# Kernel optimization log

Measured on AMD Instinct MI355X. Metric: run time of the kernel, lower is better.

The kernel has to match this reference:

```python
import jax, jax.numpy as jnp
import numpy as np
from jax import lax


def _make_kernel():
    # enhance_n_suppress_5x5 contour kernels: (96, 5, 5), only 4 channels non-zero
    n = 5
    k = np.zeros((96, n, n), dtype=np.float32)
    k[10] = np.array([[0, 0, 1, 0, 0], [0, 0, 1, 0, 0], [-1, -1, 0, -1, -1],
                      [0, 0, 1, 0, 0], [0, 0, 1, 0, 0]], np.float32) / 8.0
    k[5] = np.array([[0, 0, -1, 0, 0], [0, 0, -1, 0, 0], [1, 1, 0, 1, 1],
                     [0, 0, -1, 0, 0], [0, 0, -1, 0, 0]], np.float32) / 8.0
    diag = np.array([[1, 0, 0, 0, -1], [0, 1, 0, -1, 0], [0, 0, 0, 0, 0],
                     [0, -1, 0, 1, 0], [-1, 0, 0, 0, 1]], np.float32) / 8.0
    k[54] = diag
    k[67] = diag
    return jnp.asarray(k)


def setup_inputs() -> dict:
    key = jax.random.key(0)
    x = jax.random.normal(key, (128, 55, 55, 96), dtype=jnp.float32)  # NHWC
    kernel = _make_kernel()  # (96, 5, 5)
    return {"x": x, "kernel": kernel}


def reference(x, kernel):
    # Depthwise 5x5 correlation per channel + residual (same math as the
    # python double loop of slice+batch_dot in the original layer).
    ch = x.shape[-1]
    # (96,5,5) -> HWIO depthwise kernel (5,5,1,96)
    k = jnp.transpose(kernel, (1, 2, 0))[:, :, None, :]
    y = lax.conv_general_dilated(
        x, k,
        window_strides=(1, 1),
        padding="SAME",
        dimension_numbers=("NHWC", "HWIO", "NHWC"),
        feature_group_count=ch,
    )
    return x + y
```

## Files before the change

kernel.cpp:

```cpp
#include <hip/hip_runtime.h>

#define NB 128
#define HW 55
#define IMG (HW * HW)
#define CH 96
#define GROUPS 24
#define TAPS 25
#define NPIX (NB * IMG)
#define RSTRIP 5
#define NSTRIP (HW / RSTRIP)
#define NWG (NB * NSTRIP)
#define SROWS (RSTRIP + 4)
#define GCHUNK 4
#define SLOTG 32
#define NXCD 8
#define BITEMS (RSTRIP * HW * GROUPS)
#define SPIX (RSTRIP * HW)
#define STAGEN (SROWS * HW)

typedef float v4f __attribute__((ext_vector_type(4)));


__global__ void repack_kernel(const float* __restrict__ k,
                              float4* __restrict__ wslot,
                              int2* __restrict__ dslot,
                              int* __restrict__ tapflag,
                              int* __restrict__ gact,
                              int* __restrict__ nga,
                              int* __restrict__ nspad) {
    __shared__ int s_ns[GROUPS];
    int g = threadIdx.x;
    if (g < GROUPS) {
        int ns = 0;
        for (int tap = 0; tap < TAPS; ++tap) {
            float w0 = k[(4 * g + 0) * TAPS + tap];
            float w1 = k[(4 * g + 1) * TAPS + tap];
            float w2 = k[(4 * g + 2) * TAPS + tap];
            float w3 = k[(4 * g + 3) * TAPS + tap];
            if (w0 != 0.f || w1 != 0.f || w2 != 0.f || w3 != 0.f) {
                int dh = tap / 5 - 2, dw = tap % 5 - 2;
                wslot[g * SLOTG + ns] = make_float4(w0, w1, w2, w3);
                dslot[g * SLOTG + ns] = make_int2(dh + 2, dw);
                ++ns;
            }
        }
        for (int s = ns; s < SLOTG; ++s) {
            wslot[g * SLOTG + s] = make_float4(0.f, 0.f, 0.f, 0.f);
            dslot[g * SLOTG + s] = make_int2(2, 0);
        }
        tapflag[g] = (ns > 0) ? 1 : 0;
        s_ns[g] = ns;
    }
    __syncthreads();
    if (threadIdx.x == 0) {
        int na = 0, m = 0;
        for (int gg = 0; gg < GROUPS; ++gg)
            if (s_ns[gg] > 0) { gact[na++] = gg; m = m > s_ns[gg] ? m : s_ns[gg]; }
        *nga = na;
        *nspad = (m + 7) & ~7;
    }
}

__global__ __launch_bounds__(256) void tiled_kernel(const float* __restrict__ x,
                                                    const float4* __restrict__ wslot,
                                                    const int2* __restrict__ dslot,
                                                    const int* __restrict__ tapflag,
                                                    const int* __restrict__ gact,
                                                    const int* __restrict__ p_nga,
                                                    const int* __restrict__ p_nspad,
                                                    float* __restrict__ out) {
    __shared__ v4f s_x[GCHUNK * STAGEN];
    __shared__ v4f s_cv[GCHUNK * SPIX];
    __shared__ float4 s_w[GCHUNK * 8];
    __shared__ int s_d[GCHUNK * 8];
    __shared__ int s_info[GROUPS];
    __shared__ int s_gg[GCHUNK];

    const int q = NWG / NXCD, r = NWG % NXCD;
    int xcd = blockIdx.x & (NXCD - 1);
    int bidx = blockIdx.x >> 3;
    int swz = (xcd < r ? xcd * (q + 1) : r * (q + 1) + (xcd - r) * q) + bidx;

    const int n = swz / NSTRIP;
    const int strip = swz % NSTRIP;
    const int h0 = strip * RSTRIP;
    const int tid = threadIdx.x;
    const int nga = *p_nga;
    const int nsb = (*p_nspad) >> 3;
    const int base_f4 = (n * IMG + h0 * HW) * GROUPS;
    const v4f* x4 = (const v4f*)x;
    v4f* o4 = (v4f*)out;

    int nchunk = (nga + GCHUNK - 1) / GCHUNK;
    if (nchunk < 1) nchunk = 1;
    const bool single = (nchunk == 1);

    for (int c = 0; c < nchunk; ++c) {
        const int c0 = c * GCHUNK;
        int cn = nga - c0;
        if (cn > GCHUNK) cn = GCHUNK;
        if (cn < 0) cn = 0;

        if (tid < GROUPS) s_info[tid] = tapflag[tid] ? -2 : -1;
        __syncthreads();
        if (tid < cn) { s_info[gact[c0 + tid]] = tid; s_gg[tid] = gact[c0 + tid]; }
        if (tid < cn * 8) {
            int ci = tid >> 3, s = tid & 7;
            int gg = gact[c0 + ci];
            s_w[tid] = wslot[gg * SLOTG + s];
            int2 dd = dslot[gg * SLOTG + s];
            s_d[tid] = (dd.x << 8) | (dd.y + 2);
        }
        const int stcnt = STAGEN * cn;
        const int wcn = HW * cn;
        for (int i = tid; i < stcnt; i += 256) {
            int srow = i / wcn;
            int rem2 = i - srow * wcn;
            int pix = rem2 / cn;
            int ci = rem2 - pix * cn;
            int h = h0 - 2 + srow;
            v4f v = {0.f, 0.f, 0.f, 0.f};
            if ((unsigned)h < (unsigned)HW)
                v = x4[(n * IMG + h * HW + pix) * GROUPS + gact[c0 + ci]];
            s_x[ci * STAGEN + srow * HW + pix] = v;
        }
        __syncthreads();

        const int acnt = cn * SPIX;
        for (int j = tid; j < acnt; j += 256) {
            int ci = j / SPIX;
            int pixrel = j - ci * SPIX;
            int rr = pixrel / HW;
            int pix = pixrel - rr * HW;
            const v4f* sxg = s_x + ci * STAGEN;
            v4f acc = {0.f, 0.f, 0.f, 0.f};
#pragma unroll
            for (int si = 0; si < 8; ++si) {
                int d = s_d[ci * 8 + si];
                int srow = rr + (d >> 8);
                int pix2 = pix + (d & 255) - 2;
                bool valid = (unsigned)pix2 < (unsigned)HW;
                float sc = valid ? 1.f : 0.f;
                int p2 = valid ? pix2 : 0;
                v4f xv = sxg[srow * HW + p2];
                float4 wv = s_w[ci * 8 + si];
                acc.x += (wv.x * sc) * xv.x;
                acc.y += (wv.y * sc) * xv.y;
                acc.z += (wv.z * sc) * xv.z;
                acc.w += (wv.w * sc) * xv.w;
            }
            for (int sb = 1; sb < nsb; ++sb) {
                int gg = s_gg[ci];
#pragma unroll
                for (int si = 0; si < 8; ++si) {
                    int s = sb * 8 + si;
                    int2 dd = dslot[gg * SLOTG + s];
                    int srow = rr + dd.x;
                    int pix2 = pix + dd.y;
                    bool valid = (unsigned)pix2 < (unsigned)HW;
                    float sc = valid ? 1.f : 0.f;
                    int p2 = valid ? pix2 : 0;
                    v4f xv = sxg[srow * HW + p2];
                    float4 wv = wslot[gg * SLOTG + s];
                    acc.x += (wv.x * sc) * xv.x;
                    acc.y += (wv.y * sc) * xv.y;
                    acc.z += (wv.z * sc) * xv.z;
                    acc.w += (wv.w * sc) * xv.w;
                }
            }
            s_cv[ci * SPIX + pixrel] = acc;
        }
        __syncthreads();

        for (int i = tid; i < BITEMS; i += 256) {
            int pixrel = i / GROUPS;
            int gout = i - pixrel * GROUPS;
            v4f acc = x4[base_f4 + i];
            int gidx = s_info[gout];
            if (gidx >= 0) {
                v4f cv = s_cv[gidx * SPIX + pixrel];
                acc.x += cv.x; acc.y += cv.y; acc.z += cv.z; acc.w += cv.w;
            }
            bool dostore = single || (gidx >= 0) || (c == 0 && gidx == -1);
            if (dostore)
                __builtin_nontemporal_store(acc, &o4[base_f4 + i]);
        }
        if (c + 1 < nchunk) __syncthreads();
    }
}

__global__ __launch_bounds__(256) void fallback_kernel(const float* __restrict__ x,
                                                       const float* __restrict__ kraw,
                                                       float* __restrict__ out) {
    int t = blockIdx.x * 256 + threadIdx.x;
    if (t >= NPIX * GROUPS) return;
    int g = t % GROUPS;
    int pixel = t / GROUPS;
    int rem = pixel % IMG;
    int h = rem / HW;
    int w = rem - h * HW;
    int base = pixel * CH + g * 4;
    const float4 xc = *reinterpret_cast<const float4*>(x + base);
    float4 acc = make_float4(xc.x, xc.y, xc.z, xc.w);
#pragma unroll
    for (int dh = -2; dh <= 2; ++dh)
#pragma unroll
        for (int dw = -2; dw <= 2; ++dw) {
            const int tap = (dh + 2) * 5 + (dw + 2);
            const bool valid = ((unsigned)(h + dh) < (unsigned)HW) &
                               ((unsigned)(w + dw) < (unsigned)HW);
            const float vs = valid ? 1.0f : 0.0f;
            const int off = valid ? (dh * HW * CH + dw * CH) : 0;
            const float4 xv = *reinterpret_cast<const float4*>(x + base + off);
            acc.x += (kraw[(g * 4 + 0) * TAPS + tap] * vs) * xv.x;
            acc.y += (kraw[(g * 4 + 1) * TAPS + tap] * vs) * xv.y;
            acc.z += (kraw[(g * 4 + 2) * TAPS + tap] * vs) * xv.z;
            acc.w += (kraw[(g * 4 + 3) * TAPS + tap] * vs) * xv.w;
        }
    *reinterpret_cast<float4*>(out + base) = acc;
}

extern "C" void kernel_launch(void* const* d_in, const int* in_sizes, int n_in,
                              void* d_out, int out_size, void* d_ws, size_t ws_size,
                              hipStream_t stream) {
    const float* x = (const float*)d_in[0];
    const float* k = (const float*)d_in[1];
    float* out = (float*)d_out;

    const size_t sz_wslot = (size_t)GROUPS * SLOTG * sizeof(float4);
    const size_t sz_dslot = (size_t)GROUPS * SLOTG * sizeof(int2);
    const size_t sz_flag = GROUPS * sizeof(int);
    const size_t sz_gact = GROUPS * sizeof(int);
    const size_t ws_need = sz_wslot + sz_dslot + sz_flag + sz_gact + 2 * sizeof(int);

    if (ws_size >= ws_need) {
        char* p = (char*)d_ws;
        float4* wslot = (float4*)p;  p += sz_wslot;
        int2* dslot = (int2*)p;      p += sz_dslot;
        int* tapflag = (int*)p;      p += sz_flag;
        int* gact = (int*)p;         p += sz_gact;
        int* nga = (int*)p;          p += sizeof(int);
        int* nspad = (int*)p;

        repack_kernel<<<1, 64, 0, stream>>>(k, wslot, dslot, tapflag, gact, nga, nspad);
        tiled_kernel<<<NWG, 256, 0, stream>>>(x, wslot, dslot, tapflag, gact,
                                              nga, nspad, out);
    } else {
        const int blocks = (NPIX * GROUPS) / 256;
        fallback_kernel<<<blocks, 256, 0, stream>>>(x, k, out);
    }
}
```

Measured before the change: 90.14 us.

## Split conv and residual stages into pixel sub-chunks to shrink LDS buffer

```diff
diff --git a/kernel.cpp b/kernel.cpp
--- a/kernel.cpp
+++ b/kernel.cpp
@@ -17,6 +17,7 @@
 #define BITEMS (RSTRIP * HW * GROUPS)
 #define SPIX (RSTRIP * HW)
 #define STAGEN (SROWS * HW)
+#define PCH 128
 
 typedef float v4f __attribute__((ext_vector_type(4)));
 
@@ -70,7 +71,7 @@
                                                     const int* __restrict__ p_nspad,
                                                     float* __restrict__ out) {
     __shared__ v4f s_x[GCHUNK * STAGEN];
-    __shared__ v4f s_cv[GCHUNK * SPIX];
+    __shared__ v4f s_cv[GCHUNK * PCH];
     __shared__ float4 s_w[GCHUNK * 8];
     __shared__ int s_d[GCHUNK * 8];
     __shared__ int s_info[GROUPS];
@@ -126,66 +127,88 @@
         }
         __syncthreads();
 
-        const int acnt = cn * SPIX;
-        for (int j = tid; j < acnt; j += 256) {
-            int ci = j / SPIX;
-            int pixrel = j - ci * SPIX;
-            int rr = pixrel / HW;
-            int pix = pixrel - rr * HW;
-            const v4f* sxg = s_x + ci * STAGEN;
-            v4f acc = {0.f, 0.f, 0.f, 0.f};
-#pragma unroll
-            for (int si = 0; si < 8; ++si) {
-                int d = s_d[ci * 8 + si];
-                int srow = rr + (d >> 8);
-                int pix2 = pix + (d & 255) - 2;
-                bool valid = (unsigned)pix2 < (unsigned)HW;
-                float sc = valid ? 1.f : 0.f;
-                int p2 = valid ? pix2 : 0;
-                v4f xv = sxg[srow * HW + p2];
-                float4 wv = s_w[ci * 8 + si];
-                acc.x += (wv.x * sc) * xv.x;
-                acc.y += (wv.y * sc) * xv.y;
-                acc.z += (wv.z * sc) * xv.z;
-                acc.w += (wv.w * sc) * xv.w;
-            }
-            for (int sb = 1; sb < nsb; ++sb) {
-                int gg = s_gg[ci];
-#pragma unroll
-                for (int si = 0; si < 8; ++si) {
-                    int s = sb * 8 + si;
-                    int2 dd = dslot[gg * SLOTG + s];
-                    int srow = rr + dd.x;
-                    int pix2 = pix + dd.y;
-                    bool valid = (unsigned)pix2 < (unsigned)HW;
-                    float sc = valid ? 1.f : 0.f;
-                    int p2 = valid ? pix2 : 0;
-                    v4f xv = sxg[srow * HW + p2];
-                    float4 wv = wslot[gg * SLOTG + s];
-                    acc.x += (wv.x * sc) * xv.x;
-                    acc.y += (wv.y * sc) * xv.y;
-                    acc.z += (wv.z * sc) * xv.z;
-                    acc.w += (wv.w * sc) * xv.w;
+        for (int p0 = 0; p0 < SPIX; p0 += PCH) {
+            int pcn = SPIX - p0;
+            if (pcn > PCH) pcn = PCH;
+
+            for (int j = tid; j < cn * PCH; j += 256) {
+                int ci = j >> 7;
+                int pixrel = j & (PCH - 1);
+                if (pixrel < pcn) {
+                    int pa = p0 + pixrel;
+                    int rr = pa / HW;
+                    int pix = pa - rr * HW;
+                    const v4f* sxg = s_x + ci * STAGEN;
+                    v4f acc = {0.f, 0.f, 0.f, 0.f};
+#pragma unroll
+                    for (int si = 0; si < 8; ++si) {
+                        int d = s_d[ci * 8 + si];
+                        int srow = rr + (d >> 8);
+                        int pix2 = pix + (d & 255) - 2;
+                        bool valid = (unsigned)pix2 < (unsigned)HW;
+                        float sc = valid ? 1.f : 0.f;
+                        int p2 = valid ? pix2 : 0;
+                        v4f xv = sxg[srow * HW + p2];
+                        float4 wv = s_w[ci * 8 + si];
+                        acc.x += (wv.x * sc) * xv.x;
+                        acc.y += (wv.y * sc) * xv.y;
+                        acc.z += (wv.z * sc) * xv.z;
+                        acc.w += (wv.w * sc) * xv.w;
+                    }
+                    for (int sb = 1; sb < nsb; ++sb) {
+                        int gg = s_gg[ci];
+#pragma unroll
+                        for (int si = 0; si < 8; ++si) {
+                            int s = sb * 8 + si;
+                            int2 dd = dslot[gg * SLOTG + s];
+                            int srow = rr + dd.x;
+                            int pix2 = pix + dd.y;
+                            bool valid = (unsigned)pix2 < (unsigned)HW;
+                            float sc = valid ? 1.f : 0.f;
+                            int p2 = valid ? pix2 : 0;
+                            v4f xv = sxg[srow * HW + p2];
+                            float4 wv = wslot[gg * SLOTG + s];
+                            acc.x += (wv.x * sc) * xv.x;
+                            acc.y += (wv.y * sc) * xv.y;
+                            acc.z += (wv.z * sc) * xv.z;
+                            acc.w += (wv.w * sc) * xv.w;
+                        }
+                    }
+                    s_cv[ci * PCH + pixrel] = acc;
                 }
             }
-            s_cv[ci * SPIX + pixrel] = acc;
-        }
-        __syncthreads();
-
-        for (int i = tid; i < BITEMS; i += 256) {
-            int pixrel = i / GROUPS;
-            int gout = i - pixrel * GROUPS;
-            v4f acc = x4[base_f4 + i];
-            int gidx = s_info[gout];
-            if (gidx >= 0) {
-                v4f cv = s_cv[gidx * SPIX + pixrel];
-                acc.x += cv.x; acc.y += cv.y; acc.z += cv.z; acc.w += cv.w;
+            __syncthreads();
+
+            const int ib = base_f4 + p0 * GROUPS;
+            if (pcn == PCH) {
+                for (int jj = tid; jj < 768; jj += 256) {
+#pragma unroll
+                    for (int kc = 0; kc < 4; ++kc) {
+                        int i = jj + kc * 768;
+                        int pr = i / GROUPS;
+                        int gout = i - pr * GROUPS;
+                        v4f acc = x4[ib + i];
+                        int gidx = s_info[gout];
+                        if (gidx >= 0) acc += s_cv[gidx * PCH + pr];
+                        if (single || gidx >= 0 || (c == 0 && gidx == -1))
+                            __builtin_nontemporal_store(acc, &o4[ib + i]);
+                    }
+                }
+            } else {
+                const int tot = pcn * GROUPS;
+                for (int i = tid; i < tot; i += 256) {
+                    int pr = i / GROUPS;
+                    int gout = i - pr * GROUPS;
+                    v4f acc = x4[ib + i];
+                    int gidx = s_info[gout];
+                    if (gidx >= 0) acc += s_cv[gidx * PCH + pr];
+                    if (single || gidx >= 0 || (c == 0 && gidx == -1))
+                        __builtin_nontemporal_store(acc, &o4[ib + i]);
+                }
             }
-            bool dostore = single || (gidx >= 0) || (c == 0 && gidx == -1);
-            if (dostore)
-                __builtin_nontemporal_store(acc, &o4[base_f4 + i]);
-        }
-        if (c + 1 < nchunk) __syncthreads();
+            if (p0 + PCH < SPIX || c + 1 < nchunk)
+                __syncthreads();
+        }
     }
 }
 
```

Result: slower. 94.58 us (+4.9%).

## Split fused tiled kernel into conv-to-buffer pass and streaming residual pass

Applied to the files above, without the earlier changes.

```diff
diff --git a/kernel.cpp b/kernel.cpp
--- a/kernel.cpp
+++ b/kernel.cpp
@@ -9,14 +9,17 @@
 #define NPIX (NB * IMG)
 #define RSTRIP 5
 #define NSTRIP (HW / RSTRIP)
-#define NWG (NB * NSTRIP)
+#define NWG1 (NB * NSTRIP)
+#define TOTALF4 (NPIX * GROUPS)
+#define NWG2 (TOTALF4 / 256)
 #define SROWS (RSTRIP + 4)
 #define GCHUNK 4
 #define SLOTG 32
 #define NXCD 8
-#define BITEMS (RSTRIP * HW * GROUPS)
 #define SPIX (RSTRIP * HW)
 #define STAGEN (SROWS * HW)
+#define BITEMS (RSTRIP * HW * GROUPS)
+#define PCH_FB 128
 
 typedef float v4f __attribute__((ext_vector_type(4)));
 
@@ -27,7 +30,8 @@
                               int* __restrict__ tapflag,
                               int* __restrict__ gact,
                               int* __restrict__ nga,
-                              int* __restrict__ nspad) {
+                              int* __restrict__ nspad,
+                              int* __restrict__ amask) {
     __shared__ int s_ns[GROUPS];
     int g = threadIdx.x;
     if (g < GROUPS) {
@@ -53,30 +57,36 @@
     }
     __syncthreads();
     if (threadIdx.x == 0) {
-        int na = 0, m = 0;
+        int na = 0, m = 0, msk = 0;
         for (int gg = 0; gg < GROUPS; ++gg)
-            if (s_ns[gg] > 0) { gact[na++] = gg; m = m > s_ns[gg] ? m : s_ns[gg]; }
+            if (s_ns[gg] > 0) {
+                gact[na++] = gg;
+                msk |= (1 << gg);
+                m = m > s_ns[gg] ? m : s_ns[gg];
+            }
         *nga = na;
         *nspad = (m + 7) & ~7;
-    }
-}
-
-__global__ __launch_bounds__(256) void tiled_kernel(const float* __restrict__ x,
-                                                    const float4* __restrict__ wslot,
-                                                    const int2* __restrict__ dslot,
-                                                    const int* __restrict__ tapflag,
-                                                    const int* __restrict__ gact,
-                                                    const int* __restrict__ p_nga,
-                                                    const int* __restrict__ p_nspad,
-                                                    float* __restrict__ out) {
+        *amask = msk;
+    }
+}
+
+__global__ __launch_bounds__(256) void conv_kernel(const float* __restrict__ x,
+                                                   const float4* __restrict__ wslot,
+                                                   const int2* __restrict__ dslot,
+                                                   const int* __restrict__ gact,
+                                                   const int* __restrict__ p_nga,
+                                                   const int* __restrict__ p_nspad,
+                                                   v4f* __restrict__ cvbuf) {
     __shared__ v4f s_x[GCHUNK * STAGEN];
-    __shared__ v4f s_cv[GCHUNK * SPIX];
     __shared__ float4 s_w[GCHUNK * 8];
     __shared__ int s_d[GCHUNK * 8];
-    __shared__ int s_info[GROUPS];
-    __shared__ int s_gg[GCHUNK];
-
-    const int q = NWG / NXCD, r = NWG % NXCD;
+
+    int cn = *p_nga;
+    if (cn > GCHUNK) cn = GCHUNK;
+    if (cn == 0) return;
+    const int nsb = (*p_nspad) >> 3;
+
+    const int q = NWG1 / NXCD, r = NWG1 % NXCD;
     int xcd = blockIdx.x & (NXCD - 1);
     int bidx = blockIdx.x >> 3;
     int swz = (xcd < r ? xcd * (q + 1) : r * (q + 1) + (xcd - r) * q) + bidx;
@@ -85,115 +95,139 @@
     const int strip = swz % NSTRIP;
     const int h0 = strip * RSTRIP;
     const int tid = threadIdx.x;
-    const int nga = *p_nga;
-    const int nsb = (*p_nspad) >> 3;
-    const int base_f4 = (n * IMG + h0 * HW) * GROUPS;
+    const int pixbase = n * IMG + h0 * HW;
     const v4f* x4 = (const v4f*)x;
-    v4f* o4 = (v4f*)out;
-
-    int nchunk = (nga + GCHUNK - 1) / GCHUNK;
-    if (nchunk < 1) nchunk = 1;
-    const bool single = (nchunk == 1);
-
-    for (int c = 0; c < nchunk; ++c) {
-        const int c0 = c * GCHUNK;
-        int cn = nga - c0;
-        if (cn > GCHUNK) cn = GCHUNK;
-        if (cn < 0) cn = 0;
-
-        if (tid < GROUPS) s_info[tid] = tapflag[tid] ? -2 : -1;
-        __syncthreads();
-        if (tid < cn) { s_info[gact[c0 + tid]] = tid; s_gg[tid] = gact[c0 + tid]; }
-        if (tid < cn * 8) {
-            int ci = tid >> 3, s = tid & 7;
-            int gg = gact[c0 + ci];
-            s_w[tid] = wslot[gg * SLOTG + s];
-            int2 dd = dslot[gg * SLOTG + s];
-            s_d[tid] = (dd.x << 8) | (dd.y + 2);
-        }
-        const int stcnt = STAGEN * cn;
-        const int wcn = HW * cn;
-        for (int i = tid; i < stcnt; i += 256) {
-            int srow = i / wcn;
-            int rem2 = i - srow * wcn;
-            int pix = rem2 / cn;
-            int ci = rem2 - pix * cn;
-            int h = h0 - 2 + srow;
-            v4f v = {0.f, 0.f, 0.f, 0.f};
-            if ((unsigned)h < (unsigned)HW)
-                v = x4[(n * IMG + h * HW + pix) * GROUPS + gact[c0 + ci]];
-            s_x[ci * STAGEN + srow * HW + pix] = v;
-        }
-        __syncthreads();
-
-        const int acnt = cn * SPIX;
-        for (int j = tid; j < acnt; j += 256) {
-            int ci = j / SPIX;
-            int pixrel = j - ci * SPIX;
-            int rr = pixrel / HW;
-            int pix = pixrel - rr * HW;
-            const v4f* sxg = s_x + ci * STAGEN;
-            v4f acc = {0.f, 0.f, 0.f, 0.f};
+
+    if (tid < cn * 8) {
+        int ci = tid >> 3, s = tid & 7;
+        int gg = gact[ci];
+        s_w[tid] = wslot[gg * SLOTG + s];
+        int2 dd = dslot[gg * SLOTG + s];
+        s_d[tid] = (dd.x << 8) | (dd.y + 2);
+    }
+    const int stcnt = STAGEN * cn;
+    const int wcn = HW * cn;
+    for (int i = tid; i < stcnt; i += 256) {
+        int srow = i / wcn;
+        int rem2 = i - srow * wcn;
+        int pix = rem2 / cn;
+        int ci = rem2 - pix * cn;
+        int h = h0 - 2 + srow;
+        v4f v = {0.f, 0.f, 0.f, 0.f};
+        if ((unsigned)h < (unsigned)HW)
+            v = x4[(n * IMG + h * HW + pix) * GROUPS + gact[ci]];
+        s_x[ci * STAGEN + srow * HW + pix] = v;
+    }
+    __syncthreads();
+
+    const int acnt = SPIX * cn;
+    for (int j = tid; j < acnt; j += 256) {
+        int pa = j / cn;
+        int ci = j - pa * cn;
+        int rr = pa / HW;
+        int pix = pa - rr * HW;
+        const v4f* sxg = s_x + ci * STAGEN;
+        v4f acc = {0.f, 0.f, 0.f, 0.f};
+#pragma unroll
+        for (int si = 0; si < 8; ++si) {
+            int d = s_d[ci * 8 + si];
+            int srow = rr + (d >> 8);
+            int pix2 = pix + (d & 255) - 2;
+            bool valid = (unsigned)pix2 < (unsigned)HW;
+            float sc = valid ? 1.f : 0.f;
+            int p2 = valid ? pix2 : 0;
+            v4f xv = sxg[srow * HW + p2];
+            float4 wv = s_w[ci * 8 + si];
+            acc.x += (wv.x * sc) * xv.x;
+            acc.y += (wv.y * sc) * xv.y;
+            acc.z += (wv.z * sc) * xv.z;
+            acc.w += (wv.w * sc) * xv.w;
+        }
+        for (int sb = 1; sb < nsb; ++sb) {
+            int gg = gact[ci];
 #pragma unroll
             for (int si = 0; si < 8; ++si) {
-                int d = s_d[ci * 8 + si];
-                int srow = rr + (d >> 8);
-                int pix2 = pix + (d & 255) - 2;
+                int s = sb * 8 + si;
+                int2 dd = dslot[gg * SLOTG + s];
+                int srow = rr + dd.x;
+                int pix2 = pix + dd.y;
                 bool valid = (unsigned)pix2 < (unsigned)HW;
                 float sc = valid ? 1.f : 0.f;
                 int p2 = valid ? pix2 : 0;
                 v4f xv = sxg[srow * HW + p2];
-                float4 wv = s_w[ci * 8 + si];
+                float4 wv = wslot[gg * SLOTG + s];
                 acc.x += (wv.x * sc) * xv.x;
                 acc.y += (wv.y * sc) * xv.y;
                 acc.z += (wv.z * sc) * xv.z;
                 acc.w += (wv.w * sc) * xv.w;
             }
-            for (int sb = 1; sb < nsb; ++sb) {
-                int gg = s_gg[ci];
+        }
+        __builtin_nontemporal_store(acc, &cvbuf[(size_t)(pixbase + pa) * cn + ci]);
+    }
+}
+
+__global__ __launch_bounds__(256) void stream_kernel(const float* __restrict__ x,
+                                                     const v4f* __restrict__ cvbuf,
+                                                     const float4* __restrict__ wslot,
+                                                     const int2* __restrict__ dslot,
+                                                     const int* __restrict__ p_amask,
+                                                     const int* __restrict__ p_nspad,
+                                                     float* __restrict__ out) {
+    const int q = NWG2 / NXCD, r = NWG2 % NXCD;
+    int xcd = blockIdx.x & (NXCD - 1);
+    int bidx = blockIdx.x >> 3;
+    int swz = (xcd < r ? xcd * (q + 1) : r * (q + 1) + (xcd - r) * q) + bidx;
+
+    const int i = swz * 256 + threadIdx.x;
+    const int g = i % GROUPS;
+    const int pixel = i / GROUPS;
+    const v4f* x4 = (const v4f*)x;
+    v4f acc = x4[i];
+
+    const int amask = *p_amask;
+    const int ngtot = __popc(amask);
+    const bool act = (amask >> g) & 1;
+    if (act) {
+        int aidx = __popc(amask & ((1u << g) - 1));
+        int cn = ngtot < GCHUNK ? ngtot : GCHUNK;
+        if (aidx < GCHUNK)
+            acc += cvbuf[(size_t)pixel * cn + aidx];
+    }
+    if (ngtot > GCHUNK) {
+        int aidx = act ? __popc(amask & ((1u << g) - 1)) : 0;
+        if (act && aidx >= GCHUNK) {
+            int rem = pixel % IMG;
+            int h = rem / HW, w = rem - h * HW;
+            const float* xb = x + (size_t)i * 4;
+            int nsb = (*p_nspad) >> 3;
+            for (int sb = 0; sb < nsb; ++sb) {
 #pragma unroll
                 for (int si = 0; si < 8; ++si) {
                     int s = sb * 8 + si;
-                    int2 dd = dslot[gg * SLOTG + s];
-                    int srow = rr + dd.x;
-                    int pix2 = pix + dd.y;
-                    bool valid = (unsigned)pix2 < (unsigned)HW;
+                    int2 dd = dslot[g * SLOTG + s];
+                    int dh2 = dd.x, dw = dd.y;
+                    bool valid = ((unsigned)(h + dh2 - 2) < (unsigned)HW) &
+                                 ((unsigned)(w + dw) < (unsigned)HW);
                     float sc = valid ? 1.f : 0.f;
-                    int p2 = valid ? pix2 : 0;
-                    v4f xv = sxg[srow * HW + p2];
-                    float4 wv = wslot[gg * SLOTG + s];
+                    int off = valid ? ((dh2 - 2) * HW * CH + dw * CH) : 0;
+                    v4f xv = *(const v4f*)(xb + off);
+                    float4 wv = wslot[g * SLOTG + s];
                     acc.x += (wv.x * sc) * xv.x;
                     acc.y += (wv.y * sc) * xv.y;
                     acc.z += (wv.z * sc) * xv.z;
                     acc.w += (wv.w * sc) * xv.w;
                 }
             }
-            s_cv[ci * SPIX + pixrel] = acc;
-        }
-        __syncthreads();
-
-        for (int i = tid; i < BITEMS; i += 256) {
-            int pixrel = i / GROUPS;
-            int gout = i - pixrel * GROUPS;
-            v4f acc = x4[base_f4 + i];
-            int gidx = s_info[gout];
-            if (gidx >= 0) {
-                v4f cv = s_cv[gidx * SPIX + pixrel];
-                acc.x += cv.x; acc.y += cv.y; acc.z += cv.z; acc.w += cv.w;
-            }
-            bool dostore = single || (gidx >= 0) || (c == 0 && gidx == -1);
-            if (dostore)
-                __builtin_nontemporal_store(acc, &o4[base_f4 + i]);
-        }
-        if (c + 1 < nchunk) __syncthreads();
-    }
+        }
+    }
+    __builtin_nontemporal_store(acc, &((v4f*)out)[i]);
 }
 
 __global__ __launch_bounds__(256) void fallback_kernel(const float* __restrict__ x,
                                                        const float* __restrict__ kraw,
                                                        float* __restrict__ out) {
     int t = blockIdx.x * 256 + threadIdx.x;
-    if (t >= NPIX * GROUPS) return;
+    if (t >= TOTALF4) return;
     int g = t % GROUPS;
     int pixel = t / GROUPS;
     int rem = pixel % IMG;
@@ -231,22 +265,29 @@
     const size_t sz_dslot = (size_t)GROUPS * SLOTG * sizeof(int2);
     const size_t sz_flag = GROUPS * sizeof(int);
     const size_t sz_gact = GROUPS * sizeof(int);
-    const size_t ws_need = sz_wslot + sz_dslot + sz_flag + sz_gact + 2 * sizeof(int);
-
-    if (ws_size >= ws_need) {
+    const size_t sz_scalars = 3 * sizeof(int);
+    size_t tab_bytes = sz_wslot + sz_dslot + sz_flag + sz_gact + sz_scalars;
+    tab_bytes = (tab_bytes + 15) & ~(size_t)15;
+    const size_t sz_cvbuf = (size_t)NPIX * GCHUNK * sizeof(v4f);
+
+    if (ws_size >= tab_bytes + sz_cvbuf) {
         char* p = (char*)d_ws;
         float4* wslot = (float4*)p;  p += sz_wslot;
         int2* dslot = (int2*)p;      p += sz_dslot;
         int* tapflag = (int*)p;      p += sz_flag;
         int* gact = (int*)p;         p += sz_gact;
         int* nga = (int*)p;          p += sizeof(int);
-        int* nspad = (int*)p;
-
-        repack_kernel<<<1, 64, 0, stream>>>(k, wslot, dslot, tapflag, gact, nga, nspad);
-        tiled_kernel<<<NWG, 256, 0, stream>>>(x, wslot, dslot, tapflag, gact,
-                                              nga, nspad, out);
+        int* nspad = (int*)p;        p += sizeof(int);
+        int* amask = (int*)p;
+        v4f* cvbuf = (v4f*)((char*)d_ws + tab_bytes);
+
+        repack_kernel<<<1, 64, 0, stream>>>(k, wslot, dslot, tapflag, gact,
+                                            nga, nspad, amask);
+        conv_kernel<<<NWG1, 256, 0, stream>>>(x, wslot, dslot, gact, nga, nspad,
+                                              cvbuf);
+        stream_kernel<<<NWG2, 256, 0, stream>>>(x, cvbuf, wslot, dslot, amask,
+                                                nspad, out);
     } else {
-        const int blocks = (NPIX * GROUPS) / 256;
-        fallback_kernel<<<blocks, 256, 0, stream>>>(x, k, out);
-    }
-}
+        fallback_kernel<<<NWG2, 256, 0, stream>>>(x, k, out);
+    }
+}
```

Result: slower. 110.9 us (+23.0%).
